# Performance work log

Hardware: AMD Instinct MI355X
Metric: run time of the kernel (lower is better)

Reference implementation:

```python
import jax, jax.numpy as jnp
import numpy as np

B, Q, K = 4, 256, 1024          # batch, query_len, key_len
DQ, DK, DV, H = 512, 512, 512, 256  # query/key/value dims, num_hiddens


def setup_inputs() -> dict:
    key = jax.random.key(0)
    ks = jax.random.split(key, 7)
    return {
        "queries": jax.random.normal(ks[0], (B, Q, DQ), jnp.float32),
        "keys": jax.random.normal(ks[1], (B, K, DK), jnp.float32),
        "values": jax.random.normal(ks[2], (B, K, DV), jnp.float32),
        "valid_lens": jax.random.randint(ks[3], (B,), 1, K + 1),
        "Wq": jax.random.normal(ks[4], (H, DQ), jnp.float32) / np.sqrt(DQ).astype(np.float32),
        "Wk": jax.random.normal(ks[5], (H, DK), jnp.float32) / np.sqrt(DK).astype(np.float32),
        "wv": jax.random.normal(ks[6], (H,), jnp.float32) / np.sqrt(H).astype(np.float32),
    }


def reference(queries, keys, values, valid_lens, Wq, Wk, wv):
    # Linear projections (bias=False), torch Linear weight layout (out, in)
    q = jnp.einsum("bqd,hd->bqh", queries, Wq)          # (B, Q, H)
    k = jnp.einsum("bkd,hd->bkh", keys, Wk)             # (B, K, H)
    # Broadcast add -> tanh -> scalar score per (q, k) pair
    feats = jnp.tanh(q[:, :, None, :] + k[:, None, :, :])  # (B, Q, K, H)
    scores = jnp.einsum("bqkh,h->bqk", feats, wv)           # (B, Q, K)
    # masked_softmax with 1D valid_lens: mask applies along key axis per batch
    kv_len = scores.shape[-1]
    mask = jnp.arange(kv_len)[None, None, :] < valid_lens[:, None, None]  # (B,1,K)
    scores = jnp.where(mask, scores, jnp.float32(-1e6))
    attn = jax.nn.softmax(scores, axis=-1)               # (B, Q, K)
    # dropout is identity in eval mode
    return jnp.einsum("bqk,bkv->bqv", attn, values)      # (B, Q, DV)
```

## Files before the change

### kernel.cpp

```cpp
#include <hip/hip_runtime.h>
#include <stdint.h>


#define NB 4
#define NQ 256
#define NK 1024
#define ND 512
#define NH 256
#define QROWS 4
#define PR 8

#define C2L2E 2.8853900817779268f
#define L2E   1.4426950408889634f

__device__ void ff_vldec(const int* p, int* v) {
  bool ok = true;
  for (int i = 0; i < 4; ++i) { int x = p[i]; if (x < 1 || x > NK) ok = false; }
  if (ok) { for (int i = 0; i < 4; ++i) v[i] = p[i]; return; }
  ok = true;
  for (int i = 0; i < 4; ++i) {
    if (p[2 * i + 1] != 0) ok = false;
    int x = p[2 * i]; if (x < 1 || x > NK) ok = false;
  }
  if (ok) { for (int i = 0; i < 4; ++i) v[i] = p[2 * i]; return; }
  ok = true;
  for (int i = 0; i < 4; ++i) {
    union { int i; float f; } u; u.i = p[i];
    if (!(u.f >= 1.0f && u.f <= 1024.0f && u.f == floorf(u.f))) ok = false;
  }
  if (ok) {
    for (int i = 0; i < 4; ++i) { union { int i; float f; } u; u.i = p[i]; v[i] = (int)u.f; }
    return;
  }
  ok = true;
  for (int i = 0; i < 4; ++i) {
    union { long long l; double d; } u;
    u.l = ((long long)p[2 * i + 1] << 32) | (unsigned int)p[2 * i];
    if (!(u.d >= 1.0 && u.d <= 1024.0 && u.d == floor(u.d))) ok = false;
  }
  if (ok) {
    for (int i = 0; i < 4; ++i) {
      union { long long l; double d; } u;
      u.l = ((long long)p[2 * i + 1] << 32) | (unsigned int)p[2 * i];
      v[i] = (int)u.d;
    }
    return;
  }
  const uint16_t* hh = (const uint16_t*)p;
  const short*    s  = (const short*)p;
  ok = true;
  for (int i = 0; i < 4; ++i) { int x = s[i]; if (x < 1 || x > NK) ok = false; }
  if (ok) { for (int i = 0; i < 4; ++i) v[i] = s[i]; return; }
  ok = true;
  for (int i = 0; i < 4; ++i) {
    union { uint16_t u; _Float16 h; } u; u.u = hh[i];
    float f = (float)u.h;
    if (!(f >= 1.0f && f <= 1024.0f && f == floorf(f))) ok = false;
  }
  if (ok) {
    for (int i = 0; i < 4; ++i) {
      union { uint16_t u; _Float16 h; } u; u.u = hh[i];
      v[i] = (int)(float)u.h;
    }
    return;
  }
  ok = true;
  for (int i = 0; i < 4; ++i) {
    union { uint32_t u; float f; } u; u.u = ((uint32_t)hh[i]) << 16;
    if (!(u.f >= 1.0f && u.f <= 1028.0f)) ok = false;
  }
  if (ok) {
    for (int i = 0; i < 4; ++i) {
      union { uint32_t u; float f; } u; u.u = ((uint32_t)hh[i]) << 16;
      int x = (int)(u.f + 0.5f); if (x > NK) x = NK; v[i] = x;
    }
    return;
  }
  for (int i = 0; i < 4; ++i) v[i] = NK;
}

__global__ __launch_bounds__(256) void ff_wt(
    const float* __restrict__ Wq, const float* __restrict__ Wk,
    float* __restrict__ WTq, float* __restrict__ WTk)
{
  const int idx = blockIdx.x * 256 + threadIdx.x;
  const int d4 = idx & 127, h = idx >> 7;
  const float* src = blockIdx.y ? Wk : Wq;
  float*       dst = blockIdx.y ? WTk : WTq;
  float4 w = *(const float4*)(src + (size_t)h * ND + d4 * 4);
  w.x *= C2L2E; w.y *= C2L2E; w.z *= C2L2E; w.w *= C2L2E;
  *(float4*)(dst + ((size_t)d4 * NH + h) * 4) = w;
}

__global__ __launch_bounds__(256) void ff_proj(
    const float* __restrict__ q_in, const float* __restrict__ k_in,
    const float* __restrict__ WTq, const float* __restrict__ WTk,
    float* __restrict__ qp, float* __restrict__ kp)
{
  const int t = threadIdx.x;
  const bool isq = blockIdx.x < (NB * NQ / PR);
  const int g = isq ? blockIdx.x : (blockIdx.x - NB * NQ / PR);
  const float* xin = (isq ? q_in : k_in) + (size_t)g * PR * ND;
  const float* WT  = isq ? WTq : WTk;

  float acc[PR];
  #pragma unroll
  for (int r = 0; r < PR; ++r) acc[r] = 0.f;

  #pragma unroll 2
  for (int d4 = 0; d4 < ND / 4; ++d4) {
    float4 w = *(const float4*)(WT + ((size_t)d4 * NH + t) * 4);
    #pragma unroll
    for (int r = 0; r < PR; ++r) {
      float4 x = *(const float4*)(xin + (size_t)r * ND + d4 * 4);
      acc[r] += w.x * x.x + w.y * x.y + w.z * x.z + w.w * x.w;
    }
  }

  if (isq) {
    float* o = qp + (size_t)g * PR * NH + t;
    #pragma unroll
    for (int r = 0; r < PR; ++r) o[(size_t)r * NH] = acc[r];
  } else {
    const int r0 = g * PR;
    const int bb = r0 >> 10, rk = r0 & (NK - 1);
    float* o = kp + ((size_t)bb * NH + t) * NK + rk;
    *(float4*)o       = make_float4(acc[0], acc[1], acc[2], acc[3]);
    *(float4*)(o + 4) = make_float4(acc[4], acc[5], acc[6], acc[7]);
  }
}

__global__ __launch_bounds__(1024) void ff_attn(
    const float* __restrict__ qp, const float* __restrict__ kp,
    const float* __restrict__ vals, const int* __restrict__ vlraw,
    const float* __restrict__ wvp, float* __restrict__ out)
{
  __shared__ float qs[NH * QROWS];
  __shared__ float ws[NH];
  __shared__ float st[NK * QROWS];
  __shared__ float pm[16], psm[16];
  __shared__ float part[4 * QROWS * ND];

  const int t  = threadIdx.x;
  const int q0 = blockIdx.x * QROWS;
  const int b  = blockIdx.y;

  {
    const float* qsrc = qp + ((size_t)b * NQ + q0) * NH;
    const int row = t >> 8, h = t & 255;
    qs[h * QROWS + row] = qsrc[t];
    if (t < NH) ws[t] = -2.0f * wvp[t];
  }
  __syncthreads();

  int vls[4];
  ff_vldec(vlraw, vls);
  const int vl = vls[b];

  float a0 = 0.f, a1 = 0.f, a2 = 0.f, a3 = 0.f;
  {
    const float* kvp = kp + (size_t)b * NH * NK + t;
    #pragma unroll 8
    for (int h = 0; h < NH; ++h) {
      float  kv = kvp[(size_t)h * NK];
      float4 q4 = *(const float4*)(qs + h * QROWS);
      float  w  = ws[h];
      a0 += w * __builtin_amdgcn_rcpf(1.0f + __builtin_amdgcn_exp2f(q4.x + kv));
      a1 += w * __builtin_amdgcn_rcpf(1.0f + __builtin_amdgcn_exp2f(q4.y + kv));
      a2 += w * __builtin_amdgcn_rcpf(1.0f + __builtin_amdgcn_exp2f(q4.z + kv));
      a3 += w * __builtin_amdgcn_rcpf(1.0f + __builtin_amdgcn_exp2f(q4.w + kv));
    }
  }
  {
    const bool ok = (t < vl);
    *(float4*)&st[t * 4] = make_float4(ok ? a0 : -1e6f, ok ? a1 : -1e6f,
                                       ok ? a2 : -1e6f, ok ? a3 : -1e6f);
  }
  __syncthreads();

  {
    const int wid = t >> 6, lane = t & 63;
    const int row = wid >> 2, seg = wid & 3;
    const int kb = seg * 256 + lane;
    float v0 = st[(kb      ) * 4 + row];
    float v1 = st[(kb +  64) * 4 + row];
    float v2 = st[(kb + 128) * 4 + row];
    float v3 = st[(kb + 192) * 4 + row];
    float m = fmaxf(fmaxf(v0, v1), fmaxf(v2, v3));
    for (int o = 32; o; o >>= 1) m = fmaxf(m, __shfl_xor(m, o));
    if (lane == 0) pm[wid] = m;
    __syncthreads();
    m = fmaxf(fmaxf(pm[row*4+0], pm[row*4+1]), fmaxf(pm[row*4+2], pm[row*4+3]));
    float e0 = __builtin_amdgcn_exp2f((v0 - m) * L2E);
    float e1 = __builtin_amdgcn_exp2f((v1 - m) * L2E);
    float e2 = __builtin_amdgcn_exp2f((v2 - m) * L2E);
    float e3 = __builtin_amdgcn_exp2f((v3 - m) * L2E);
    float sm = e0 + e1 + e2 + e3;
    for (int o = 32; o; o >>= 1) sm += __shfl_xor(sm, o);
    if (lane == 0) psm[wid] = sm;
    __syncthreads();
    const float S = psm[row*4+0] + psm[row*4+1] + psm[row*4+2] + psm[row*4+3];
    const float rr = 1.0f / S;
    st[(kb      ) * 4 + row] = e0 * rr;
    st[(kb +  64) * 4 + row] = e1 * rr;
    st[(kb + 128) * 4 + row] = e2 * rr;
    st[(kb + 192) * 4 + row] = e3 * rr;
  }
  __syncthreads();

  {
    const int kq = t >> 8, c2 = (t & 255) * 2;
    const float* vb = vals + (size_t)b * NK * ND + c2;
    float ox0=0.f, oy0=0.f, ox1=0.f, oy1=0.f;
    float ox2=0.f, oy2=0.f, ox3=0.f, oy3=0.f;
    const int k0 = kq * 256;
    #pragma unroll 8
    for (int k = k0; k < k0 + 256; ++k) {
      float2 v2 = *(const float2*)(vb + (size_t)k * ND);
      float4 a  = *(const float4*)&st[k * 4];
      ox0 += a.x * v2.x; oy0 += a.x * v2.y;
      ox1 += a.y * v2.x; oy1 += a.y * v2.y;
      ox2 += a.z * v2.x; oy2 += a.z * v2.y;
      ox3 += a.w * v2.x; oy3 += a.w * v2.y;
    }
    float* pp = &part[(size_t)kq * QROWS * ND + c2];
    *(float2*)(pp         ) = make_float2(ox0, oy0);
    *(float2*)(pp +     ND) = make_float2(ox1, oy1);
    *(float2*)(pp + 2 * ND) = make_float2(ox2, oy2);
    *(float2*)(pp + 3 * ND) = make_float2(ox3, oy3);
  }
  __syncthreads();
  {
    const int r = t >> 8, c2 = (t & 255) * 2;
    const float* pp = &part[(size_t)r * ND + c2];
    float2 s = make_float2(0.f, 0.f);
    #pragma unroll
    for (int kq = 0; kq < 4; ++kq) {
      float2 p = *(const float2*)(pp + (size_t)kq * QROWS * ND);
      s.x += p.x; s.y += p.y;
    }
    *(float2*)(out + ((size_t)b * NQ + q0 + r) * ND + c2) = s;
  }
}

extern "C" void kernel_launch(void* const* d_in, const int* in_sizes, int n_in,
                              void* d_out, int out_size, void* d_ws, size_t ws_size,
                              hipStream_t stream) {
  const float* queries = (const float*)d_in[0];
  const float* keys    = (const float*)d_in[1];
  const float* values  = (const float*)d_in[2];
  const int*   vlens   = (const int*)d_in[3];
  const float* Wq      = (const float*)d_in[4];
  const float* Wk      = (const float*)d_in[5];
  const float* wv      = (const float*)d_in[6];
  float* out = (float*)d_out;

  float* qp  = (float*)d_ws;
  float* kp  = qp  + (size_t)NB * NQ * NH;
  float* wtq = kp  + (size_t)NB * NH * NK;
  float* wtk = wtq + (size_t)(ND / 4) * NH * 4;

  ff_wt  <<<dim3(128, 2), 256, 0, stream>>>(Wq, Wk, wtq, wtk);
  ff_proj<<<dim3(NB * NQ / PR + NB * NK / PR), 256, 0, stream>>>(
      queries, keys, wtq, wtk, qp, kp);
  ff_attn<<<dim3(NQ / QROWS, NB), 1024, 0, stream>>>(qp, kp, values, vlens, wv, out);
}
```

Baseline: 209.6 us.

## Skip masked keys, drop softmax max pass, retile projection with LDS staging

The attention kernel skips score computation for wavefronts whose keys are all beyond the valid length, and limits the value accumulation to valid keys. Softmax drops the max-reduction pass, relying on bounded tanh-based scores, and folds normalization into the final partial sums, which removes two barriers. The projection kernel stages input rows in shared memory and uses a 4x2 register tile with a reorganized weight layout. Dropping the max subtraction assumes the scores stay small enough that exp does not overflow.

```diff
diff --git a/kernel.cpp b/kernel.cpp
--- a/kernel.cpp
+++ b/kernel.cpp
@@ -8,7 +8,6 @@
 #define ND 512
 #define NH 256
 #define QROWS 4
-#define PR 8
 
 #define C2L2E 2.8853900817779268f
 #define L2E   1.4426950408889634f
@@ -89,7 +88,7 @@
   float*       dst = blockIdx.y ? WTk : WTq;
   float4 w = *(const float4*)(src + (size_t)h * ND + d4 * 4);
   w.x *= C2L2E; w.y *= C2L2E; w.z *= C2L2E; w.w *= C2L2E;
-  *(float4*)(dst + ((size_t)d4 * NH + h) * 4) = w;
+  *(float4*)(dst + ((size_t)d4 * 64 + (h >> 2)) * 16 + (h & 3) * 4) = w;
 }
 
 __global__ __launch_bounds__(256) void ff_proj(
@@ -97,36 +96,48 @@
     const float* __restrict__ WTq, const float* __restrict__ WTk,
     float* __restrict__ qp, float* __restrict__ kp)
 {
+  __shared__ float xs[8 * ND];
   const int t = threadIdx.x;
-  const bool isq = blockIdx.x < (NB * NQ / PR);
-  const int g = isq ? blockIdx.x : (blockIdx.x - NB * NQ / PR);
-  const float* xin = (isq ? q_in : k_in) + (size_t)g * PR * ND;
+  const bool isq = blockIdx.x < (NB * NQ / 8);
+  const int g = isq ? blockIdx.x : (blockIdx.x - NB * NQ / 8);
+  const float* xin = (isq ? q_in : k_in) + (size_t)g * 8 * ND;
   const float* WT  = isq ? WTq : WTk;
 
-  float acc[PR];
   #pragma unroll
-  for (int r = 0; r < PR; ++r) acc[r] = 0.f;
-
+  for (int i = 0; i < 4; ++i)
+    ((float4*)xs)[t + 256 * i] = ((const float4*)xin)[t + 256 * i];
+  __syncthreads();
+
+  const int hg = t & 63, rg = t >> 6;
+  float ac[4][2];
+  #pragma unroll
+  for (int j = 0; j < 4; ++j) { ac[j][0] = 0.f; ac[j][1] = 0.f; }
+
+  const float* wbase = WT + (size_t)hg * 16;
   #pragma unroll 2
   for (int d4 = 0; d4 < ND / 4; ++d4) {
-    float4 w = *(const float4*)(WT + ((size_t)d4 * NH + t) * 4);
+    const float* wp = wbase + (size_t)d4 * 64 * 16;
+    float4 x0 = *(const float4*)&xs[(2 * rg    ) * ND + d4 * 4];
+    float4 x1 = *(const float4*)&xs[(2 * rg + 1) * ND + d4 * 4];
     #pragma unroll
-    for (int r = 0; r < PR; ++r) {
-      float4 x = *(const float4*)(xin + (size_t)r * ND + d4 * 4);
-      acc[r] += w.x * x.x + w.y * x.y + w.z * x.z + w.w * x.w;
+    for (int j = 0; j < 4; ++j) {
+      float4 w = *(const float4*)(wp + j * 4);
+      ac[j][0] += w.x*x0.x + w.y*x0.y + w.z*x0.z + w.w*x0.w;
+      ac[j][1] += w.x*x1.x + w.y*x1.y + w.z*x1.z + w.w*x1.w;
     }
   }
 
   if (isq) {
-    float* o = qp + (size_t)g * PR * NH + t;
+    float* o = qp + ((size_t)g * 8) * NH;
+    *(float4*)(o + (size_t)(2*rg    ) * NH + 4*hg) = make_float4(ac[0][0], ac[1][0], ac[2][0], ac[3][0]);
+    *(float4*)(o + (size_t)(2*rg + 1) * NH + 4*hg) = make_float4(ac[0][1], ac[1][1], ac[2][1], ac[3][1]);
+  } else {
+    const int r0 = g * 8;
+    const int bb = r0 >> 10, rk = r0 & (NK - 1);
+    float* o = kp + ((size_t)bb * NH + 4*hg) * NK + rk + 2*rg;
     #pragma unroll
-    for (int r = 0; r < PR; ++r) o[(size_t)r * NH] = acc[r];
-  } else {
-    const int r0 = g * PR;
-    const int bb = r0 >> 10, rk = r0 & (NK - 1);
-    float* o = kp + ((size_t)bb * NH + t) * NK + rk;
-    *(float4*)o       = make_float4(acc[0], acc[1], acc[2], acc[3]);
-    *(float4*)(o + 4) = make_float4(acc[4], acc[5], acc[6], acc[7]);
+    for (int j = 0; j < 4; ++j)
+      *(float2*)(o + (size_t)j * NK) = make_float2(ac[j][0], ac[j][1]);
   }
 }
 
@@ -138,7 +149,7 @@
   __shared__ float qs[NH * QROWS];
   __shared__ float ws[NH];
   __shared__ float st[NK * QROWS];
-  __shared__ float pm[16], psm[16];
+  __shared__ float psum[16 * 4];
   __shared__ float part[4 * QROWS * ND];
 
   const int t  = threadIdx.x;
@@ -158,7 +169,7 @@
   const int vl = vls[b];
 
   float a0 = 0.f, a1 = 0.f, a2 = 0.f, a3 = 0.f;
-  {
+  if ((t & ~63) < vl) {
     const float* kvp = kp + (size_t)b * NH * NK + t;
     #pragma unroll 8
     for (int h = 0; h < NH; ++h) {
@@ -171,71 +182,63 @@
       a3 += w * __builtin_amdgcn_rcpf(1.0f + __builtin_amdgcn_exp2f(q4.w + kv));
     }
   }
-  {
-    const bool ok = (t < vl);
-    *(float4*)&st[t * 4] = make_float4(ok ? a0 : -1e6f, ok ? a1 : -1e6f,
-                                       ok ? a2 : -1e6f, ok ? a3 : -1e6f);
-  }
-  __syncthreads();
-
-  {
-    const int wid = t >> 6, lane = t & 63;
-    const int row = wid >> 2, seg = wid & 3;
-    const int kb = seg * 256 + lane;
-    float v0 = st[(kb      ) * 4 + row];
-    float v1 = st[(kb +  64) * 4 + row];
-    float v2 = st[(kb + 128) * 4 + row];
-    float v3 = st[(kb + 192) * 4 + row];
-    float m = fmaxf(fmaxf(v0, v1), fmaxf(v2, v3));
-    for (int o = 32; o; o >>= 1) m = fmaxf(m, __shfl_xor(m, o));
-    if (lane == 0) pm[wid] = m;
-    __syncthreads();
-    m = fmaxf(fmaxf(pm[row*4+0], pm[row*4+1]), fmaxf(pm[row*4+2], pm[row*4+3]));
-    float e0 = __builtin_amdgcn_exp2f((v0 - m) * L2E);
-    float e1 = __builtin_amdgcn_exp2f((v1 - m) * L2E);
-    float e2 = __builtin_amdgcn_exp2f((v2 - m) * L2E);
-    float e3 = __builtin_amdgcn_exp2f((v3 - m) * L2E);
-    float sm = e0 + e1 + e2 + e3;
-    for (int o = 32; o; o >>= 1) sm += __shfl_xor(sm, o);
-    if (lane == 0) psm[wid] = sm;
-    __syncthreads();
-    const float S = psm[row*4+0] + psm[row*4+1] + psm[row*4+2] + psm[row*4+3];
-    const float rr = 1.0f / S;
-    st[(kb      ) * 4 + row] = e0 * rr;
-    st[(kb +  64) * 4 + row] = e1 * rr;
-    st[(kb + 128) * 4 + row] = e2 * rr;
-    st[(kb + 192) * 4 + row] = e3 * rr;
-  }
-  __syncthreads();
+  float e0, e1, e2, e3;
+  {
+    const bool okm = (t < vl);
+    e0 = okm ? __builtin_amdgcn_exp2f(a0 * L2E) : 0.f;
+    e1 = okm ? __builtin_amdgcn_exp2f(a1 * L2E) : 0.f;
+    e2 = okm ? __builtin_amdgcn_exp2f(a2 * L2E) : 0.f;
+    e3 = okm ? __builtin_amdgcn_exp2f(a3 * L2E) : 0.f;
+    *(float4*)&st[t * 4] = make_float4(e0, e1, e2, e3);
+    float s0 = e0, s1 = e1, s2 = e2, s3 = e3;
+    for (int o = 32; o; o >>= 1) {
+      s0 += __shfl_xor(s0, o); s1 += __shfl_xor(s1, o);
+      s2 += __shfl_xor(s2, o); s3 += __shfl_xor(s3, o);
+    }
+    if ((t & 63) == 0)
+      *(float4*)&psum[(t >> 6) * 4] = make_float4(s0, s1, s2, s3);
+  }
+  __syncthreads();
+
+  float4 S = make_float4(0.f, 0.f, 0.f, 0.f);
+  #pragma unroll
+  for (int w = 0; w < 16; ++w) {
+    float4 p = *(const float4*)&psum[w * 4];
+    S.x += p.x; S.y += p.y; S.z += p.z; S.w += p.w;
+  }
+  const float r0 = 1.0f / S.x, r1 = 1.0f / S.y, r2 = 1.0f / S.z, r3 = 1.0f / S.w;
 
   {
     const int kq = t >> 8, c2 = (t & 255) * 2;
-    const float* vb = vals + (size_t)b * NK * ND + c2;
-    float ox0=0.f, oy0=0.f, ox1=0.f, oy1=0.f;
-    float ox2=0.f, oy2=0.f, ox3=0.f, oy3=0.f;
     const int k0 = kq * 256;
-    #pragma unroll 8
-    for (int k = k0; k < k0 + 256; ++k) {
-      float2 v2 = *(const float2*)(vb + (size_t)k * ND);
-      float4 a  = *(const float4*)&st[k * 4];
-      ox0 += a.x * v2.x; oy0 += a.x * v2.y;
-      ox1 += a.y * v2.x; oy1 += a.y * v2.y;
-      ox2 += a.z * v2.x; oy2 += a.z * v2.y;
-      ox3 += a.w * v2.x; oy3 += a.w * v2.y;
-    }
-    float* pp = &part[(size_t)kq * QROWS * ND + c2];
-    *(float2*)(pp         ) = make_float2(ox0, oy0);
-    *(float2*)(pp +     ND) = make_float2(ox1, oy1);
-    *(float2*)(pp + 2 * ND) = make_float2(ox2, oy2);
-    *(float2*)(pp + 3 * ND) = make_float2(ox3, oy3);
-  }
-  __syncthreads();
-  {
+    if (k0 < vl) {
+      const int kend = (k0 + 256 < vl) ? k0 + 256 : vl;
+      const float* vb = vals + (size_t)b * NK * ND + c2;
+      float ox0=0.f, oy0=0.f, ox1=0.f, oy1=0.f;
+      float ox2=0.f, oy2=0.f, ox3=0.f, oy3=0.f;
+      #pragma unroll 8
+      for (int k = k0; k < kend; ++k) {
+        float2 v2 = *(const float2*)(vb + (size_t)k * ND);
+        float4 a  = *(const float4*)&st[k * 4];
+        ox0 += a.x * v2.x; oy0 += a.x * v2.y;
+        ox1 += a.y * v2.x; oy1 += a.y * v2.y;
+        ox2 += a.z * v2.x; oy2 += a.z * v2.y;
+        ox3 += a.w * v2.x; oy3 += a.w * v2.y;
+      }
+      float* pp = &part[(size_t)kq * QROWS * ND + c2];
+      *(float2*)(pp         ) = make_float2(ox0 * r0, oy0 * r0);
+      *(float2*)(pp +     ND) = make_float2(ox1 * r1, oy1 * r1);
+      *(float2*)(pp + 2 * ND) = make_float2(ox2 * r2, oy2 * r2);
+      *(float2*)(pp + 3 * ND) = make_float2(ox3 * r3, oy3 * r3);
+    }
+  }
+  __syncthreads();
+  {
+    const int nq = (vl + 255) >> 8;
     const int r = t >> 8, c2 = (t & 255) * 2;
     const float* pp = &part[(size_t)r * ND + c2];
     float2 s = make_float2(0.f, 0.f);
-    #pragma unroll
-    for (int kq = 0; kq < 4; ++kq) {
+    for (int kq = 0; kq < nq; ++kq) {
       float2 p = *(const float2*)(pp + (size_t)kq * QROWS * ND);
       s.x += p.x; s.y += p.y;
     }
@@ -261,7 +264,7 @@
   float* wtk = wtq + (size_t)(ND / 4) * NH * 4;
 
   ff_wt  <<<dim3(128, 2), 256, 0, stream>>>(Wq, Wk, wtq, wtk);
-  ff_proj<<<dim3(NB * NQ / PR + NB * NK / PR), 256, 0, stream>>>(
+  ff_proj<<<dim3(NB * NQ / 8 + NB * NK / 8), 256, 0, stream>>>(
       queries, keys, wtq, wtk, qp, kp);
   ff_attn<<<dim3(NQ / QROWS, NB), 1024, 0, stream>>>(qp, kp, values, vlens, wv, out);
 }
```

Result: slower. 277.0 us (+32.2%).
